# Optimization experiments

Measured on AMD Instinct MI355X. Metric: run time of the kernel, lower is better.

## Reference

```python
import jax, jax.numpy as jnp
import numpy as np

N_NODES = 100000
N_EDGES = 1600000
N_GRAPHS = 64
IN_DIM, HID_DIM, OUT_DIM = 128, 256, 256


def setup_inputs() -> dict:
    key = jax.random.key(0)
    ks = jax.random.split(key, 7)
    x = jax.random.normal(ks[0], (N_NODES, IN_DIM), dtype=jnp.float32)
    edge_index = jax.random.randint(ks[1], (2, N_EDGES), 0, N_NODES, dtype=jnp.int32)
    batch = jnp.sort(jax.random.randint(ks[2], (N_NODES,), 0, N_GRAPHS, dtype=jnp.int32))
    # Glorot-style init for GCN linear weights, zero bias (as in PyG defaults)
    W1 = jax.random.normal(ks[3], (IN_DIM, HID_DIM), dtype=jnp.float32) / np.sqrt(IN_DIM)
    b1 = jnp.zeros((HID_DIM,), dtype=jnp.float32)
    W2 = jax.random.normal(ks[4], (HID_DIM, OUT_DIM), dtype=jnp.float32) / np.sqrt(HID_DIM)
    b2 = jnp.zeros((OUT_DIM,), dtype=jnp.float32)
    return {"x": x, "edge_index": edge_index, "batch": batch,
            "W1": W1, "b1": b1, "W2": W2, "b2": b2}


def reference(x, edge_index, batch, W1, b1, W2, b2):
    N = x.shape[0]
    # --- GCN normalization with self-loops (computed once, edge structure fixed) ---
    loops = jnp.arange(N, dtype=edge_index.dtype)
    row = jnp.concatenate([edge_index[0], loops])  # source nodes  [E+N]
    col = jnp.concatenate([edge_index[1], loops])  # target nodes  [E+N]
    deg = jax.ops.segment_sum(jnp.ones_like(col, dtype=x.dtype), col, num_segments=N)
    dinv = jax.lax.rsqrt(jnp.maximum(deg, 1.0))    # deg >= 1 due to self-loops
    norm = dinv[row] * dinv[col]                   # [E+N]

    def gcn_conv(h, W, b):
        h = h @ W                                  # linear transform first (PyG order)
        msg = h[row] * norm[:, None]               # gather + normalize  [E+N, D]
        agg = jax.ops.segment_sum(msg, col, num_segments=N)  # scatter-add
        return agg + b

    h = jax.nn.relu(gcn_conv(x, W1, b1))
    h = jax.nn.relu(gcn_conv(h, W2, b2))

    # --- global mean pool over graph ids ---
    s = jax.ops.segment_sum(h, batch, num_segments=N_GRAPHS)           # [G, D]
    cnt = jax.ops.segment_sum(jnp.ones((N, 1), h.dtype), batch, num_segments=N_GRAPHS)
    return s / jnp.maximum(cnt, 1.0)
```

## Files before the change

kernel.cpp:

```cpp
#include <hip/hip_runtime.h>

typedef __attribute__((ext_vector_type(8))) short short8;
typedef __attribute__((ext_vector_type(4))) float float4v;
typedef __attribute__((ext_vector_type(4))) uint uint4v;

#define CAP 64
#define NREP 8

__device__ __forceinline__ ushort f2bf(float f) {
    uint u = __float_as_uint(f);
    u += 0x7fffu + ((u >> 16) & 1u);
    return (ushort)(u >> 16);
}
__device__ __forceinline__ float bf2f(ushort h) {
    return __uint_as_float((uint)h << 16);
}
__device__ __forceinline__ void acc8(float* acc, uint4 v) {
    acc[0] += __uint_as_float(v.x << 16);
    acc[1] += __uint_as_float(v.x & 0xffff0000u);
    acc[2] += __uint_as_float(v.y << 16);
    acc[3] += __uint_as_float(v.y & 0xffff0000u);
    acc[4] += __uint_as_float(v.z << 16);
    acc[5] += __uint_as_float(v.z & 0xffff0000u);
    acc[6] += __uint_as_float(v.w << 16);
    acc[7] += __uint_as_float(v.w & 0xffff0000u);
}
__device__ __forceinline__ int clampi(int v, int n) {
    return (int)min((uint)v, (uint)(n - 1));
}

__global__ void zero_all_k(int* __restrict__ cnt, float* __restrict__ out,
                           int ncnt, int nout) {
    int i = blockIdx.x * 256 + threadIdx.x;
    if (i < ncnt) cnt[i] = 0;
    if (i < nout) out[i] = 0.f;
}

__global__ void countW_k(const int* __restrict__ col, int* __restrict__ cnt,
                         unsigned char* __restrict__ rank, int E, int N, int ebl,
                         const float* __restrict__ W1, ushort* __restrict__ W1p,
                         const float* __restrict__ W2, ushort* __restrict__ W2p) {
    int b = blockIdx.x;
    if (b < ebl) {
        int e = b * 256 + threadIdx.x;
        int r = b & (NREP - 1);
        if (e < E) {
            int c = col[e];
            int p = atomicAdd(&cnt[(size_t)r * N + c], 1);
            rank[e] = (unsigned char)min(p, 255);
        }
    } else {
        int idx = (b - ebl) * 256 + threadIdx.x;
        if (idx < 32768) {
            int j = idx & 7, lane = (idx >> 3) & 63;
            int s = (idx >> 9) % 4, nt = (idx >> 9) / 4;
            int k = 32 * s + (lane >> 4) * 8 + j;
            int c = nt * 16 + (lane & 15);
            W1p[idx] = f2bf(W1[k * 256 + c]);
        } else if (idx < 32768 + 65536) {
            int q = idx - 32768;
            int j = q & 7, lane = (q >> 3) & 63;
            int s = (q >> 9) % 8, nt = (q >> 9) / 8;
            int k = 32 * s + (lane >> 4) * 8 + j;
            int c = nt * 16 + (lane & 15);
            W2p[q] = f2bf(W2[k * 256 + c]);
        }
    }
}

__global__ void scan_k(const int* __restrict__ cnt, int* __restrict__ idg,
                       unsigned long long* __restrict__ bases, int N) {
    int v = blockIdx.x * 256 + threadIdx.x;
    if (v >= N) return;
    int deg = 0;
    unsigned long long pk = 0;
#pragma unroll
    for (int r = 0; r < NREP; ++r) {
        pk |= (unsigned long long)min(deg, 255) << (8 * r);
        deg += cnt[(size_t)r * N + v];
    }
    idg[v] = deg;
    bases[v] = pk;
}

__global__ void placeC_k(const int* __restrict__ row, const int* __restrict__ col,
                         const unsigned char* __restrict__ rank,
                         const unsigned long long* __restrict__ bases,
                         int* __restrict__ eidx, int E, int ebl,
                         const float* __restrict__ x, const int* __restrict__ idg,
                         ushort* __restrict__ xb, int n4) {
    int b = blockIdx.x;
    if (b < ebl) {
        int e = b * 256 + threadIdx.x;
        int r = b & (NREP - 1);
        if (e < E) {
            int c = col[e];
            int slot = (int)((bases[c] >> (8 * r)) & 255) + (int)rank[e];
            if (slot < CAP) eidx[(size_t)c * CAP + slot] = row[e];
        }
    } else {
        int i = (b - ebl) * 256 + threadIdx.x;
        if (i < n4) {
            int node = i >> 5;
            float di = rsqrtf((float)(idg[node] + 1));
            float4 v = ((const float4*)x)[i];
            ushort4 o;
            o.x = f2bf(v.x * di); o.y = f2bf(v.y * di);
            o.z = f2bf(v.z * di); o.w = f2bf(v.w * di);
            ((ushort4*)xb)[i] = o;
        }
    }
}

__global__ __launch_bounds__(256) void agg128_k(const ushort* __restrict__ g,
                                                ushort* __restrict__ out,
                                                const int* __restrict__ idg,
                                                const int* __restrict__ eidx, int n) {
    int w = threadIdx.x >> 6, lane = threadIdx.x & 63;
    int q = lane >> 4, sub = lane & 15;
    int i = blockIdx.x * 16 + w * 4 + q;
    if (i >= n) return;
    const ushort* gp = g + (size_t)sub * 8;
    float acc[8] = {};
    {
        uint4 v = *(const uint4*)(gp + (size_t)i * 128);
        acc8(acc, v);
    }
    int deg = idg[i];
    int cnt = min(deg, CAP);
    const int* ep = eidx + (size_t)i * CAP;
    int j = 0;
    for (; j + 8 <= cnt; j += 8) {
        int s0 = clampi(__builtin_nontemporal_load(ep + j), n);
        int s1 = clampi(__builtin_nontemporal_load(ep + j + 1), n);
        int s2 = clampi(__builtin_nontemporal_load(ep + j + 2), n);
        int s3 = clampi(__builtin_nontemporal_load(ep + j + 3), n);
        int s4 = clampi(__builtin_nontemporal_load(ep + j + 4), n);
        int s5 = clampi(__builtin_nontemporal_load(ep + j + 5), n);
        int s6 = clampi(__builtin_nontemporal_load(ep + j + 6), n);
        int s7 = clampi(__builtin_nontemporal_load(ep + j + 7), n);
        uint4 v0 = *(const uint4*)(gp + (size_t)s0 * 128);
        uint4 v1 = *(const uint4*)(gp + (size_t)s1 * 128);
        uint4 v2 = *(const uint4*)(gp + (size_t)s2 * 128);
        uint4 v3 = *(const uint4*)(gp + (size_t)s3 * 128);
        uint4 v4 = *(const uint4*)(gp + (size_t)s4 * 128);
        uint4 v5 = *(const uint4*)(gp + (size_t)s5 * 128);
        uint4 v6 = *(const uint4*)(gp + (size_t)s6 * 128);
        uint4 v7 = *(const uint4*)(gp + (size_t)s7 * 128);
        acc8(acc, v0); acc8(acc, v1); acc8(acc, v2); acc8(acc, v3);
        acc8(acc, v4); acc8(acc, v5); acc8(acc, v6); acc8(acc, v7);
    }
    if (j + 4 <= cnt) {
        int s0 = clampi(__builtin_nontemporal_load(ep + j), n);
        int s1 = clampi(__builtin_nontemporal_load(ep + j + 1), n);
        int s2 = clampi(__builtin_nontemporal_load(ep + j + 2), n);
        int s3 = clampi(__builtin_nontemporal_load(ep + j + 3), n);
        uint4 v0 = *(const uint4*)(gp + (size_t)s0 * 128);
        uint4 v1 = *(const uint4*)(gp + (size_t)s1 * 128);
        uint4 v2 = *(const uint4*)(gp + (size_t)s2 * 128);
        uint4 v3 = *(const uint4*)(gp + (size_t)s3 * 128);
        acc8(acc, v0); acc8(acc, v1); acc8(acc, v2); acc8(acc, v3);
        j += 4;
    }
    if (j + 2 <= cnt) {
        int s0 = clampi(__builtin_nontemporal_load(ep + j), n);
        int s1 = clampi(__builtin_nontemporal_load(ep + j + 1), n);
        uint4 v0 = *(const uint4*)(gp + (size_t)s0 * 128);
        uint4 v1 = *(const uint4*)(gp + (size_t)s1 * 128);
        acc8(acc, v0); acc8(acc, v1);
        j += 2;
    }
    if (j < cnt) {
        int s0 = clampi(__builtin_nontemporal_load(ep + j), n);
        uint4 v0 = *(const uint4*)(gp + (size_t)s0 * 128);
        acc8(acc, v0);
    }
    float di = rsqrtf((float)(deg + 1));
    uint4v o;
    o.x = (uint)f2bf(acc[0] * di) | ((uint)f2bf(acc[1] * di) << 16);
    o.y = (uint)f2bf(acc[2] * di) | ((uint)f2bf(acc[3] * di) << 16);
    o.z = (uint)f2bf(acc[4] * di) | ((uint)f2bf(acc[5] * di) << 16);
    o.w = (uint)f2bf(acc[6] * di) | ((uint)f2bf(acc[7] * di) << 16);
    __builtin_nontemporal_store(o, (uint4v*)(out + (size_t)i * 128 + sub * 8));
}

__global__ __launch_bounds__(256) void agg256_k(const ushort* __restrict__ g,
                                                ushort* __restrict__ out,
                                                const int* __restrict__ idg,
                                                const int* __restrict__ eidx, int n) {
    int w = threadIdx.x >> 6, lane = threadIdx.x & 63;
    int half = lane >> 5, sub = lane & 31;
    int i = blockIdx.x * 8 + w * 2 + half;
    if (i >= n) return;
    const ushort* gp = g + (size_t)sub * 8;
    float acc[8] = {};
    {
        uint4 v = *(const uint4*)(gp + (size_t)i * 256);
        acc8(acc, v);
    }
    int deg = idg[i];
    int cnt = min(deg, CAP);
    const int* ep = eidx + (size_t)i * CAP;
    int j = 0;
    for (; j + 8 <= cnt; j += 8) {
        int s0 = clampi(__builtin_nontemporal_load(ep + j), n);
        int s1 = clampi(__builtin_nontemporal_load(ep + j + 1), n);
        int s2 = clampi(__builtin_nontemporal_load(ep + j + 2), n);
        int s3 = clampi(__builtin_nontemporal_load(ep + j + 3), n);
        int s4 = clampi(__builtin_nontemporal_load(ep + j + 4), n);
        int s5 = clampi(__builtin_nontemporal_load(ep + j + 5), n);
        int s6 = clampi(__builtin_nontemporal_load(ep + j + 6), n);
        int s7 = clampi(__builtin_nontemporal_load(ep + j + 7), n);
        uint4 v0 = *(const uint4*)(gp + (size_t)s0 * 256);
        uint4 v1 = *(const uint4*)(gp + (size_t)s1 * 256);
        uint4 v2 = *(const uint4*)(gp + (size_t)s2 * 256);
        uint4 v3 = *(const uint4*)(gp + (size_t)s3 * 256);
        uint4 v4 = *(const uint4*)(gp + (size_t)s4 * 256);
        uint4 v5 = *(const uint4*)(gp + (size_t)s5 * 256);
        uint4 v6 = *(const uint4*)(gp + (size_t)s6 * 256);
        uint4 v7 = *(const uint4*)(gp + (size_t)s7 * 256);
        acc8(acc, v0); acc8(acc, v1); acc8(acc, v2); acc8(acc, v3);
        acc8(acc, v4); acc8(acc, v5); acc8(acc, v6); acc8(acc, v7);
    }
    if (j + 4 <= cnt) {
        int s0 = clampi(__builtin_nontemporal_load(ep + j), n);
        int s1 = clampi(__builtin_nontemporal_load(ep + j + 1), n);
        int s2 = clampi(__builtin_nontemporal_load(ep + j + 2), n);
        int s3 = clampi(__builtin_nontemporal_load(ep + j + 3), n);
        uint4 v0 = *(const uint4*)(gp + (size_t)s0 * 256);
        uint4 v1 = *(const uint4*)(gp + (size_t)s1 * 256);
        uint4 v2 = *(const uint4*)(gp + (size_t)s2 * 256);
        uint4 v3 = *(const uint4*)(gp + (size_t)s3 * 256);
        acc8(acc, v0); acc8(acc, v1); acc8(acc, v2); acc8(acc, v3);
        j += 4;
    }
    if (j + 2 <= cnt) {
        int s0 = clampi(__builtin_nontemporal_load(ep + j), n);
        int s1 = clampi(__builtin_nontemporal_load(ep + j + 1), n);
        uint4 v0 = *(const uint4*)(gp + (size_t)s0 * 256);
        uint4 v1 = *(const uint4*)(gp + (size_t)s1 * 256);
        acc8(acc, v0); acc8(acc, v1);
        j += 2;
    }
    if (j < cnt) {
        int s0 = clampi(__builtin_nontemporal_load(ep + j), n);
        uint4 v0 = *(const uint4*)(gp + (size_t)s0 * 256);
        acc8(acc, v0);
    }
    float di = rsqrtf((float)(deg + 1));
    uint4v o;
    o.x = (uint)f2bf(acc[0] * di) | ((uint)f2bf(acc[1] * di) << 16);
    o.y = (uint)f2bf(acc[2] * di) | ((uint)f2bf(acc[3] * di) << 16);
    o.z = (uint)f2bf(acc[4] * di) | ((uint)f2bf(acc[5] * di) << 16);
    o.w = (uint)f2bf(acc[6] * di) | ((uint)f2bf(acc[7] * di) << 16);
    __builtin_nontemporal_store(o, (uint4v*)(out + (size_t)i * 256 + sub * 8));
}

template <int K, bool SCALE>
__global__ __launch_bounds__(256) void gemm_ldsw_k(const ushort* __restrict__ A,
                                                   const ushort* __restrict__ Wp,
                                                   const float* __restrict__ bias,
                                                   const int* __restrict__ idg,
                                                   ushort* __restrict__ C, int M) {
    constexpr int S = K / 32;
    constexpr int STAGE_US = 4 * S * 64 * 8;
    __shared__ ushort ldsW[STAGE_US];
    int tid = threadIdx.x, wv = tid >> 6, lane = tid & 63;
    int quad = lane >> 4, l15 = lane & 15;
    int rowBase = blockIdx.x * 64 + wv * 16;
    int arow = rowBase + l15; if (arow > M - 1) arow = M - 1;
    const ushort* abase = A + (size_t)arow * K + quad * 8;
    short8 af[S];
#pragma unroll
    for (int s = 0; s < S; ++s) af[s] = *(const short8*)(abase + 32 * s);

    float diRow[4];
    if (SCALE) {
#pragma unroll
        for (int r = 0; r < 4; ++r) {
            int rr = min(rowBase + quad * 4 + r, M - 1);
            diRow[r] = rsqrtf((float)(idg[rr] + 1));
        }
    }

#pragma unroll
    for (int st = 0; st < 4; ++st) {
        __syncthreads();
        {
            const uint4* src = (const uint4*)(Wp + (size_t)st * STAGE_US);
            uint4* dst = (uint4*)ldsW;
#pragma unroll
            for (int it = 0; it < STAGE_US / 8 / 256; ++it)
                dst[it * 256 + tid] = src[it * 256 + tid];
        }
        __syncthreads();
        float4v acc[4];
#pragma unroll
        for (int nt = 0; nt < 4; ++nt) {
            float4v a = {0.f, 0.f, 0.f, 0.f};
#pragma unroll
            for (int s = 0; s < S; ++s) {
                short8 bf = *(const short8*)&ldsW[((nt * S + s) * 64 + lane) * 8];
                a = __builtin_amdgcn_mfma_f32_16x16x32_bf16(af[s], bf, a, 0, 0, 0);
            }
            acc[nt] = a;
        }
#pragma unroll
        for (int nt = 0; nt < 4; ++nt) {
            int col = (st * 4 + nt) * 16 + l15;
            float b = bias[col];
#pragma unroll
            for (int r = 0; r < 4; ++r) {
                int rw = rowBase + quad * 4 + r;
                if (rw < M) {
                    float v = fmaxf(acc[nt][r] + b, 0.f);
                    if (SCALE) v *= diRow[r];
                    C[(size_t)rw * 256 + col] = f2bf(v);
                }
            }
        }
    }
}

__global__ void pool_k(const ushort* __restrict__ h, const int* __restrict__ batch,
                       float* __restrict__ outsum, int n) {
    int d = threadIdx.x;
    int n0 = blockIdx.x * 128;
    int n1 = min(n0 + 128, n);
    int gcur = -1;
    float sum = 0.f;
    int nn = n0;
    for (; nn + 4 <= n1; nn += 4) {
        int gs0 = batch[nn] & 63,     gs1 = batch[nn + 1] & 63;
        int gs2 = batch[nn + 2] & 63, gs3 = batch[nn + 3] & 63;
        float v0 = bf2f(h[(size_t)nn * 256 + d]);
        float v1 = bf2f(h[(size_t)(nn + 1) * 256 + d]);
        float v2 = bf2f(h[(size_t)(nn + 2) * 256 + d]);
        float v3 = bf2f(h[(size_t)(nn + 3) * 256 + d]);
        int gs[4] = {gs0, gs1, gs2, gs3};
        float vs[4] = {v0, v1, v2, v3};
#pragma unroll
        for (int t = 0; t < 4; ++t) {
            if (gs[t] != gcur) {
                if (gcur >= 0) atomicAdd(&outsum[gcur * 256 + d], sum);
                gcur = gs[t];
                sum = vs[t];
            } else {
                sum += vs[t];
            }
        }
    }
    for (; nn < n1; ++nn) {
        int g = batch[nn] & 63;
        float v = bf2f(h[(size_t)nn * 256 + d]);
        if (g != gcur) {
            if (gcur >= 0) atomicAdd(&outsum[gcur * 256 + d], sum);
            gcur = g;
            sum = v;
        } else {
            sum += v;
        }
    }
    if (gcur >= 0) atomicAdd(&outsum[gcur * 256 + d], sum);
}

__global__ void final_k(float* __restrict__ out, const int* __restrict__ batch, int n) {
    __shared__ float cntS;
    int g = blockIdx.x, d = threadIdx.x;
    if (d == 0) {
        int lo = 0, hi = n;
        while (lo < hi) { int mid = (lo + hi) >> 1; if (batch[mid] < g) lo = mid + 1; else hi = mid; }
        int s = lo;
        lo = 0; hi = n;
        int g1 = g + 1;
        while (lo < hi) { int mid = (lo + hi) >> 1; if (batch[mid] < g1) lo = mid + 1; else hi = mid; }
        cntS = (float)(lo - s);
    }
    __syncthreads();
    out[g * 256 + d] /= fmaxf(cntS, 1.0f);
}

extern "C" void kernel_launch(void* const* d_in, const int* in_sizes, int n_in,
                              void* d_out, int out_size, void* d_ws, size_t ws_size,
                              hipStream_t stream) {
    const float* x  = (const float*)d_in[0];
    const int*   ei = (const int*)d_in[1];
    const int*   batch = (const int*)d_in[2];
    const float* W1 = (const float*)d_in[3];
    const float* b1 = (const float*)d_in[4];
    const float* W2 = (const float*)d_in[5];
    const float* b2 = (const float*)d_in[6];
    float* out = (float*)d_out;

    const int N  = in_sizes[2];
    const int E  = in_sizes[1] / 2;
    const int* row = ei;
    const int* col = ei + E;

    char* p = (char*)d_ws;
    auto alloc = [&](size_t bytes) {
        char* q = p;
        p += (bytes + 255) & ~(size_t)255;
        return q;
    };
    int*    idg    = (int*)alloc((size_t)N * 4);
    int*    eidx   = (int*)alloc((size_t)N * CAP * 4);
    ushort* W1p    = (ushort*)alloc(16 * 4 * 64 * 8 * 2);
    ushort* W2p    = (ushort*)alloc(16 * 8 * 64 * 8 * 2);
    ushort* xb     = (ushort*)alloc((size_t)N * 128 * 2);
    ushort* aggX   = (ushort*)alloc((size_t)N * 128 * 2);
    ushort* g1     = (ushort*)alloc((size_t)N * 256 * 2);
    ushort* aggH   = (ushort*)alloc((size_t)N * 256 * 2);
    ushort* h2     = (ushort*)alloc((size_t)N * 256 * 2);
    int*    cnt    = (int*)alloc((size_t)NREP * N * 4);
    unsigned char* rank = (unsigned char*)alloc((size_t)E);
    unsigned long long* bases = (unsigned long long*)alloc((size_t)N * 8);

    const int ncnt = NREP * N;
    const int zb  = (ncnt + 255) / 256;
    const int nb  = (N + 255) / 256;
    const int ebl = (E + 255) / 256;
    const int n4  = N * 32;
    const int cvtb = (n4 + 255) / 256;
    const int wpb  = 98304 / 256;

    zero_all_k<<<zb, 256, 0, stream>>>(cnt, out, ncnt, out_size);

    countW_k<<<ebl + wpb, 256, 0, stream>>>(col, cnt, rank, E, N, ebl,
                                            W1, W1p, W2, W2p);
    scan_k<<<nb, 256, 0, stream>>>(cnt, idg, bases, N);
    placeC_k<<<ebl + cvtb, 256, 0, stream>>>(row, col, rank, bases, eidx, E, ebl,
                                             x, idg, xb, n4);

    agg128_k<<<(N + 15) / 16, 256, 0, stream>>>(xb, aggX, idg, eidx, N);
    const int gb = (N + 63) / 64;
    gemm_ldsw_k<128, true><<<gb, 256, 0, stream>>>(aggX, W1p, b1, idg, g1, N);

    agg256_k<<<(N + 7) / 8, 256, 0, stream>>>(g1, aggH, idg, eidx, N);
    gemm_ldsw_k<256, false><<<gb, 256, 0, stream>>>(aggH, W2p, b2, nullptr, h2, N);

    pool_k<<<(N + 127) / 128, 256, 0, stream>>>(h2, batch, out, N);
    final_k<<<64, 256, 0, stream>>>(out, batch, N);
}
```

Measured before the change: 496.2 us.

## Fuse second GCN GEMM with mean pooling via per-block partial sums

The second-layer GEMM now applies bias and ReLU and reduces rows straight into per-block, per-graph partial sums in LDS. Rows are grouped by their offset from the block's first graph id, and offsets of four or more go to a global spill buffer through atomics. A final kernel adds the partial sums that overlap each graph, plus the spill, and divides by the node count. This removes writing and re-reading the full bf16 hidden matrix and the separate pool kernel. Separately, a hipMemsetAsync clears the counters and the spill buffer in place of the custom zeroing kernel. The cost is extra LDS atomics and shuffles in the GEMM epilogue.

```diff
diff --git a/kernel.cpp b/kernel.cpp
--- a/kernel.cpp
+++ b/kernel.cpp
@@ -27,13 +27,6 @@
 }
 __device__ __forceinline__ int clampi(int v, int n) {
     return (int)min((uint)v, (uint)(n - 1));
-}
-
-__global__ void zero_all_k(int* __restrict__ cnt, float* __restrict__ out,
-                           int ncnt, int nout) {
-    int i = blockIdx.x * 256 + threadIdx.x;
-    if (i < ncnt) cnt[i] = 0;
-    if (i < nout) out[i] = 0.f;
 }
 
 __global__ void countW_k(const int* __restrict__ col, int* __restrict__ cnt,
@@ -322,62 +315,114 @@
     }
 }
 
-__global__ void pool_k(const ushort* __restrict__ h, const int* __restrict__ batch,
-                       float* __restrict__ outsum, int n) {
-    int d = threadIdx.x;
-    int n0 = blockIdx.x * 128;
-    int n1 = min(n0 + 128, n);
-    int gcur = -1;
-    float sum = 0.f;
-    int nn = n0;
-    for (; nn + 4 <= n1; nn += 4) {
-        int gs0 = batch[nn] & 63,     gs1 = batch[nn + 1] & 63;
-        int gs2 = batch[nn + 2] & 63, gs3 = batch[nn + 3] & 63;
-        float v0 = bf2f(h[(size_t)nn * 256 + d]);
-        float v1 = bf2f(h[(size_t)(nn + 1) * 256 + d]);
-        float v2 = bf2f(h[(size_t)(nn + 2) * 256 + d]);
-        float v3 = bf2f(h[(size_t)(nn + 3) * 256 + d]);
-        int gs[4] = {gs0, gs1, gs2, gs3};
-        float vs[4] = {v0, v1, v2, v3};
-#pragma unroll
-        for (int t = 0; t < 4; ++t) {
-            if (gs[t] != gcur) {
-                if (gcur >= 0) atomicAdd(&outsum[gcur * 256 + d], sum);
-                gcur = gs[t];
-                sum = vs[t];
+__global__ __launch_bounds__(256) void gemm_pool_k(const ushort* __restrict__ A,
+                                                   const ushort* __restrict__ Wp,
+                                                   const float* __restrict__ bias,
+                                                   const int* __restrict__ batch,
+                                                   float* __restrict__ psum,
+                                                   float* __restrict__ spill, int M) {
+    constexpr int S = 8;
+    constexpr int STAGE_US = 4 * S * 64 * 8;
+    __shared__ ushort ldsW[STAGE_US];
+    __shared__ float ldsSum[4][256];
+    int tid = threadIdx.x, wv = tid >> 6, lane = tid & 63;
+    int quad = lane >> 4, l15 = lane & 15;
+    int rowBase = blockIdx.x * 64 + wv * 16;
+    int arow = rowBase + l15; if (arow > M - 1) arow = M - 1;
+    const ushort* abase = A + (size_t)arow * 256 + quad * 8;
+    short8 af[S];
+#pragma unroll
+    for (int s = 0; s < S; ++s) af[s] = *(const short8*)(abase + 32 * s);
+
+    int b0 = batch[blockIdx.x * 64];
+    int sg[4];
+#pragma unroll
+    for (int r = 0; r < 4; ++r) {
+        int rw = rowBase + quad * 4 + r;
+        sg[r] = (rw < M) ? (batch[rw] - b0) : -1;
+    }
+    bool tFast = (sg[0] == sg[1]) && (sg[1] == sg[2]) && (sg[2] == sg[3]) &&
+                 sg[0] >= 0 && sg[0] < 4;
+    int sw = __builtin_amdgcn_readfirstlane(sg[0]);
+    bool waveFast = __all(tFast && (sg[0] == sw));
+
+    for (int z = tid; z < 1024; z += 256) ((float*)ldsSum)[z] = 0.f;
+
+#pragma unroll
+    for (int st = 0; st < 4; ++st) {
+        __syncthreads();
+        {
+            const uint4* src = (const uint4*)(Wp + (size_t)st * STAGE_US);
+            uint4* dst = (uint4*)ldsW;
+#pragma unroll
+            for (int it = 0; it < STAGE_US / 8 / 256; ++it)
+                dst[it * 256 + tid] = src[it * 256 + tid];
+        }
+        __syncthreads();
+        float4v acc[4];
+#pragma unroll
+        for (int nt = 0; nt < 4; ++nt) {
+            float4v a = {0.f, 0.f, 0.f, 0.f};
+#pragma unroll
+            for (int s = 0; s < S; ++s) {
+                short8 bf = *(const short8*)&ldsW[((nt * S + s) * 64 + lane) * 8];
+                a = __builtin_amdgcn_mfma_f32_16x16x32_bf16(af[s], bf, a, 0, 0, 0);
+            }
+            acc[nt] = a;
+        }
+#pragma unroll
+        for (int nt = 0; nt < 4; ++nt) {
+            int col = (st * 4 + nt) * 16 + l15;
+            float b = bias[col];
+            if (waveFast) {
+                float v = fmaxf(acc[nt][0] + b, 0.f) + fmaxf(acc[nt][1] + b, 0.f)
+                        + fmaxf(acc[nt][2] + b, 0.f) + fmaxf(acc[nt][3] + b, 0.f);
+                v += __shfl_xor(v, 16);
+                v += __shfl_xor(v, 32);
+                if (quad == 0) atomicAdd(&ldsSum[sw][col], v);
             } else {
-                sum += vs[t];
+#pragma unroll
+                for (int r = 0; r < 4; ++r) {
+                    if (sg[r] >= 0) {
+                        float v = fmaxf(acc[nt][r] + b, 0.f);
+                        if (sg[r] < 4) atomicAdd(&ldsSum[sg[r]][col], v);
+                        else atomicAdd(&spill[(b0 + sg[r]) * 256 + col], v);
+                    }
+                }
             }
         }
     }
-    for (; nn < n1; ++nn) {
-        int g = batch[nn] & 63;
-        float v = bf2f(h[(size_t)nn * 256 + d]);
-        if (g != gcur) {
-            if (gcur >= 0) atomicAdd(&outsum[gcur * 256 + d], sum);
-            gcur = g;
-            sum = v;
-        } else {
-            sum += v;
-        }
-    }
-    if (gcur >= 0) atomicAdd(&outsum[gcur * 256 + d], sum);
-}
-
-__global__ void final_k(float* __restrict__ out, const int* __restrict__ batch, int n) {
-    __shared__ float cntS;
+    __syncthreads();
+#pragma unroll
+    for (int s2 = 0; s2 < 4; ++s2)
+        psum[((size_t)blockIdx.x * 4 + s2) * 256 + tid] = ldsSum[s2][tid];
+}
+
+__global__ void final2_k(float* __restrict__ out, const float* __restrict__ psum,
+                         const float* __restrict__ spill,
+                         const int* __restrict__ batch, int n) {
+    __shared__ int sSE[2];
     int g = blockIdx.x, d = threadIdx.x;
     if (d == 0) {
         int lo = 0, hi = n;
         while (lo < hi) { int mid = (lo + hi) >> 1; if (batch[mid] < g) lo = mid + 1; else hi = mid; }
-        int s = lo;
-        lo = 0; hi = n;
-        int g1 = g + 1;
+        sSE[0] = lo;
+        lo = 0; hi = n; int g1 = g + 1;
         while (lo < hi) { int mid = (lo + hi) >> 1; if (batch[mid] < g1) lo = mid + 1; else hi = mid; }
-        cntS = (float)(lo - s);
+        sSE[1] = lo;
     }
     __syncthreads();
-    out[g * 256 + d] /= fmaxf(cntS, 1.0f);
+    int s = sSE[0], e = sSE[1];
+    float sum = spill[g * 256 + d];
+    if (e > s) {
+        int bA = s >> 6, bB = (e - 1) >> 6;
+        for (int b = bA; b <= bB; ++b) {
+            int seg = g - batch[b * 64];
+            if (seg >= 0 && seg < 4)
+                sum += psum[((size_t)b * 4 + seg) * 256 + d];
+        }
+    }
+    out[g * 256 + d] = sum / fmaxf((float)(e - s), 1.f);
 }
 
 extern "C" void kernel_launch(void* const* d_in, const int* in_sizes, int n_in,
@@ -411,20 +456,20 @@
     ushort* aggX   = (ushort*)alloc((size_t)N * 128 * 2);
     ushort* g1     = (ushort*)alloc((size_t)N * 256 * 2);
     ushort* aggH   = (ushort*)alloc((size_t)N * 256 * 2);
-    ushort* h2     = (ushort*)alloc((size_t)N * 256 * 2);
     int*    cnt    = (int*)alloc((size_t)NREP * N * 4);
+    float*  spill  = (float*)alloc(64 * 256 * 4);
     unsigned char* rank = (unsigned char*)alloc((size_t)E);
     unsigned long long* bases = (unsigned long long*)alloc((size_t)N * 8);
-
-    const int ncnt = NREP * N;
-    const int zb  = (ncnt + 255) / 256;
+    const int gb = (N + 63) / 64;
+    float*  psum   = (float*)alloc((size_t)gb * 4 * 256 * 4);
+
     const int nb  = (N + 255) / 256;
     const int ebl = (E + 255) / 256;
     const int n4  = N * 32;
     const int cvtb = (n4 + 255) / 256;
     const int wpb  = 98304 / 256;
 
-    zero_all_k<<<zb, 256, 0, stream>>>(cnt, out, ncnt, out_size);
+    hipMemsetAsync(cnt, 0, (size_t)NREP * N * 4 + 64 * 256 * 4, stream);
 
     countW_k<<<ebl + wpb, 256, 0, stream>>>(col, cnt, rank, E, N, ebl,
                                             W1, W1p, W2, W2p);
@@ -433,12 +478,10 @@
                                              x, idg, xb, n4);
 
     agg128_k<<<(N + 15) / 16, 256, 0, stream>>>(xb, aggX, idg, eidx, N);
-    const int gb = (N + 63) / 64;
     gemm_ldsw_k<128, true><<<gb, 256, 0, stream>>>(aggX, W1p, b1, idg, g1, N);
 
     agg256_k<<<(N + 7) / 8, 256, 0, stream>>>(g1, aggH, idg, eidx, N);
-    gemm_ldsw_k<256, false><<<gb, 256, 0, stream>>>(aggH, W2p, b2, nullptr, h2, N);
-
-    pool_k<<<(N + 127) / 128, 256, 0, stream>>>(h2, batch, out, N);
-    final_k<<<64, 256, 0, stream>>>(out, batch, N);
-}
+    gemm_pool_k<<<gb, 256, 0, stream>>>(aggH, W2p, b2, batch, psum, spill, N);
+
+    final2_k<<<64, 256, 0, stream>>>(out, psum, spill, batch, N);
+}
```

After: 479.9 us. 1.03x faster.
